# Kernel tuning notes

Hardware: AMD Instinct MI355X
Metric: run time of the kernel (lower is better)

## Reference

```python
import jax, jax.numpy as jnp
import numpy as np

B, S, D = 2, 4096, 768
H, DH = 12, 64
W = 256          # one-sided window (attention_window=512 // 2)
G = 8            # number of global tokens (first G positions)
NEG = -1e9


def setup_inputs() -> dict:
    key = jax.random.key(0)
    ks = jax.random.split(key, 8)
    hidden_states = jax.random.normal(ks[0], (B, S, D), dtype=jnp.float32)
    attention_mask = jnp.ones((B, S), dtype=jnp.float32)
    sc = 0.02
    Wq = jax.random.normal(ks[1], (D, D), dtype=jnp.float32) * sc
    Wk = jax.random.normal(ks[2], (D, D), dtype=jnp.float32) * sc
    Wv = jax.random.normal(ks[3], (D, D), dtype=jnp.float32) * sc
    Wqg = jax.random.normal(ks[4], (D, D), dtype=jnp.float32) * sc
    Wkg = jax.random.normal(ks[5], (D, D), dtype=jnp.float32) * sc
    Wvg = jax.random.normal(ks[6], (D, D), dtype=jnp.float32) * sc
    return {"hidden_states": hidden_states, "attention_mask": attention_mask,
            "Wq": Wq, "Wk": Wk, "Wv": Wv, "Wqg": Wqg, "Wkg": Wkg, "Wvg": Wvg}


def _heads(x):  # [B,S,D] -> [B,H,S,DH]
    return x.reshape(B, S, H, DH).transpose(0, 2, 1, 3)


def longformer_attn(hidden_states, attention_mask, Wq, Wk, Wv, Wqg, Wkg, Wvg):
    scale = 1.0 / jnp.sqrt(jnp.float32(DH))
    q = _heads(hidden_states @ Wq) * scale   # [B,H,S,DH]
    k = _heads(hidden_states @ Wk)
    v = _heads(hidden_states @ Wv)

    n = S // W                                # number of query chunks
    kp = jnp.pad(k, ((0, 0), (0, 0), (W, W), (0, 0)))
    vp = jnp.pad(v, ((0, 0), (0, 0), (W, W), (0, 0)))
    # window indices into padded seq: chunk i covers keys [i*W - W, i*W + 2W)
    idx = jnp.arange(n)[:, None] * W + jnp.arange(3 * W)[None, :]   # [n,3W]
    k_win = kp[:, :, idx]                     # [B,H,n,3W,DH]
    v_win = vp[:, :, idx]
    qc = q.reshape(B, H, n, W, DH)

    scores = jnp.einsum('bhnqd,bhnkd->bhnqk', qc, k_win)  # [B,H,n,W,3W]

    # masks: band (|key-query|<=W), valid key position, not a global key,
    # and key attention_mask
    rel = jnp.arange(3 * W)[None, :] - jnp.arange(W)[:, None]   # [W,3W] = k - q
    band = (rel >= 0) & (rel <= 2 * W)
    key_pos = idx - W                                           # [n,3W] real positions
    valid = (key_pos >= 0) & (key_pos < S) & (key_pos >= G)
    struct_mask = band[None, :, :] & valid[:, None, :]          # [n,W,3W]
    amp = jnp.pad(attention_mask, ((0, 0), (W, W)))
    am_win = amp[:, idx] > 0.5                                  # [B,n,3W]
    full_mask = struct_mask[None] & am_win[:, :, None, :]       # [B,n,W,3W]
    scores = jnp.where(full_mask[:, None], scores, NEG)

    # every query also attends to the G global keys (regular key projection)
    gk = k[:, :, :G]                                            # [B,H,G,DH]
    gscore = jnp.einsum('bhsd,bhgd->bhsg', q, gk).reshape(B, H, n, W, G)
    all_scores = jnp.concatenate([gscore, scores], axis=-1)     # [B,H,n,W,G+3W]
    probs = jax.nn.softmax(all_scores, axis=-1)

    gv = v[:, :, :G]
    out = (jnp.einsum('bhnqk,bhnkd->bhnqd', probs[..., G:], v_win)
           + jnp.einsum('bhnqg,bhgd->bhnqd', probs[..., :G], gv))
    out = out.reshape(B, H, S, DH)

    # global queries attend to ALL tokens with the *_global projections
    qg = _heads(hidden_states @ Wqg)[:, :, :G] * scale          # [B,H,G,DH]
    kg = _heads(hidden_states @ Wkg)
    vg = _heads(hidden_states @ Wvg)
    gs = jnp.einsum('bhgd,bhsd->bhgs', qg, kg)                  # [B,H,G,S]
    gs = jnp.where(attention_mask[:, None, None, :] > 0.5, gs, NEG)
    gp = jax.nn.softmax(gs, axis=-1)
    gout = jnp.einsum('bhgs,bhsd->bhgd', gp, vg)
    out = out.at[:, :, :G].set(gout)

    return out.transpose(0, 2, 1, 3).reshape(B, S, D)


def reference(hidden_states, attention_mask, Wq, Wk, Wv, Wqg, Wkg, Wvg):
    return longformer_attn(hidden_states, attention_mask, Wq, Wk, Wv, Wqg, Wkg, Wvg)
```

## Files before the change

### kernel.cpp

```cpp
#include <hip/hip_runtime.h>

#define B_ 2
#define S_ 4096
#define D_ 768
#define H_ 12
#define DH_ 64
#define W_ 256
#define G_ 8
#define NEG_ (-1e9f)
#define NC_ 64
#define CK_ 64
#define WQB 128
#define NT_ 11

typedef __attribute__((ext_vector_type(4))) float f32x4;
typedef __attribute__((ext_vector_type(16))) float f32x16;
typedef __attribute__((ext_vector_type(8))) short s16x8;
typedef __attribute__((ext_vector_type(4))) short s16x4;
typedef unsigned short ushort_t;

__device__ __forceinline__ unsigned short f2bf(float f) {
    union { float f; unsigned u; } v; v.f = f;
    unsigned r = v.u + 0x7FFFu + ((v.u >> 16) & 1u);
    return (unsigned short)(r >> 16);
}
__device__ __forceinline__ float bf2f(unsigned short b) {
    union { unsigned u; float f; } v; v.u = ((unsigned)b) << 16;
    return v.f;
}
__device__ __forceinline__ unsigned cvtpk_bf16(float lo, float hi) {
    unsigned r;
    asm("v_cvt_pk_bf16_f32 %0, %1, %2" : "=v"(r) : "v"(lo), "v"(hi));
    return r;
}
__device__ __forceinline__ void gload16(const ushort_t* g, ushort_t* l) {
    __builtin_amdgcn_global_load_lds(
        (const __attribute__((address_space(1))) unsigned*)g,
        (__attribute__((address_space(3))) unsigned*)l, 16, 0, 0);
}

__global__ __launch_bounds__(256) void convert_hs(const float* __restrict__ x,
                                                  ushort_t* __restrict__ y, int n8) {
    int i = blockIdx.x * 256 + threadIdx.x;
    if (i >= n8) return;
    float4 a = *(const float4*)&x[(size_t)i * 8];
    float4 c = *(const float4*)&x[(size_t)i * 8 + 4];
    s16x8 o;
    o[0] = (short)f2bf(a.x); o[1] = (short)f2bf(a.y);
    o[2] = (short)f2bf(a.z); o[3] = (short)f2bf(a.w);
    o[4] = (short)f2bf(c.x); o[5] = (short)f2bf(c.y);
    o[6] = (short)f2bf(c.z); o[7] = (short)f2bf(c.w);
    *(s16x8*)&y[(size_t)i * 8] = o;
}

__global__ __launch_bounds__(256) void convert_wt(const float* __restrict__ W0,
                                                  const float* __restrict__ W1,
                                                  const float* __restrict__ W2,
                                                  const float* __restrict__ W3,
                                                  const float* __restrict__ W4,
                                                  ushort_t* __restrict__ wt) {
    __shared__ float tile[32][33];
    const int w = blockIdx.z;
    const float* Wsrc = (w == 0) ? W0 : (w == 1) ? W1 : (w == 2) ? W2 : (w == 3) ? W3 : W4;
    const float scl = (w == 0) ? 0.125f * 1.44269504f : 1.0f;
    const int k0 = blockIdx.x * 32;
    const int n0 = blockIdx.y * 32;
    const int t = threadIdx.x;
    const int r = t >> 3, c4 = (t & 7) * 4;
    float4 src = *(const float4*)&Wsrc[(size_t)(k0 + r) * D_ + n0 + c4];
    tile[r][c4 + 0] = src.x; tile[r][c4 + 1] = src.y;
    tile[r][c4 + 2] = src.z; tile[r][c4 + 3] = src.w;
    __syncthreads();
    s16x4 o;
    o[0] = (short)f2bf(tile[c4 + 0][r] * scl);
    o[1] = (short)f2bf(tile[c4 + 1][r] * scl);
    o[2] = (short)f2bf(tile[c4 + 2][r] * scl);
    o[3] = (short)f2bf(tile[c4 + 3][r] * scl);
    *(s16x4*)&wt[((size_t)(w * D_ + n0 + r)) * D_ + k0 + c4] = o;
}

__global__ __launch_bounds__(256, 2) void proj_mfma(const ushort_t* __restrict__ A,
                                                    const ushort_t* __restrict__ Bt,
                                                    ushort_t* __restrict__ oq,
                                                    ushort_t* __restrict__ ok,
                                                    ushort_t* __restrict__ ov,
                                                    ushort_t* __restrict__ okg,
                                                    ushort_t* __restrict__ ovg) {
    __shared__ char smem[34048];
    ushort_t* Al = (ushort_t*)smem;
    ushort_t* Bl = Al + 128 * 64;

    const int t = threadIdx.x;
    const int m0 = blockIdx.x * 128;
    const int n0 = blockIdx.y * 128;
    const int lane = t & 63;
    const int w = t >> 6;
    const int wm = (w >> 1) * 64, wn = (w & 1) * 64;
    const int ln = lane & 15, hi = lane >> 4;

    const int srow_in_call = lane >> 3;
    const int scol = ((lane & 7) ^ srow_in_call) * 8;

    f32x4 acc[4][4];
#pragma unroll
    for (int mi = 0; mi < 4; ++mi)
#pragma unroll
        for (int ni = 0; ni < 4; ++ni) acc[mi][ni] = (f32x4){0.f, 0.f, 0.f, 0.f};

    for (int k0 = 0; k0 < D_; k0 += 64) {
        __syncthreads();
#pragma unroll
        for (int j = 0; j < 4; ++j) {
            const int rbase = (w * 4 + j) * 8;
            const int row = rbase + srow_in_call;
            gload16(&A[(size_t)(m0 + row) * D_ + k0 + scol], &Al[rbase * 64]);
            gload16(&Bt[(size_t)(n0 + row) * D_ + k0 + scol], &Bl[rbase * 64]);
        }
        __syncthreads();

#pragma unroll
        for (int ks = 0; ks < 2; ++ks) {
            s16x8 af[4], bf[4];
#pragma unroll
            for (int i = 0; i < 4; ++i) {
                const int ar = wm + i * 16 + ln;
                const int br = wn + i * 16 + ln;
                const int slot = (4 * ks + hi) ^ (ln & 7);
                af[i] = *(const s16x8*)&Al[ar * 64 + slot * 8];
                bf[i] = *(const s16x8*)&Bl[br * 64 + slot * 8];
            }
#pragma unroll
            for (int mi = 0; mi < 4; ++mi)
#pragma unroll
                for (int ni = 0; ni < 4; ++ni)
                    acc[mi][ni] = __builtin_amdgcn_mfma_f32_16x16x32_bf16(af[mi], bf[ni], acc[mi][ni], 0, 0, 0);
        }
    }

    float* scr = (float*)smem;
    const int rl = t >> 2, cs = (t & 3) * 32;
    const int ng = n0 + cs;
    const int w_idx = ng / D_;
    const int cb = ng - w_idx * D_;
    const int hh = cb >> 6, dd = cb & 63;
    ushort_t* dst = (w_idx == 0) ? oq : (w_idx == 1) ? ok : (w_idx == 2) ? ov
                    : (w_idx == 3) ? okg : ovg;

#pragma unroll
    for (int r = 0; r < 2; ++r) {
        __syncthreads();
        if ((w >> 1) == r) {
#pragma unroll
            for (int mi = 0; mi < 4; ++mi)
#pragma unroll
                for (int ni = 0; ni < 4; ++ni)
#pragma unroll
                    for (int rr = 0; rr < 4; ++rr)
                        scr[(mi * 16 + hi * 4 + rr) * 132 + wn + ni * 16 + ln] = acc[mi][ni][rr];
        }
        __syncthreads();
        const int m = m0 + r * 64 + rl;
        const int bb = m >> 12, s = m & 4095;
        ushort_t* drow = dst + ((size_t)(bb * H_ + hh) * S_ + s) * DH_ + dd;
        const float* srcp = scr + rl * 132 + cs;
#pragma unroll
        for (int seg = 0; seg < 4; ++seg) {
            float4 lo = *(const float4*)&srcp[seg * 8];
            float4 hi4 = *(const float4*)&srcp[seg * 8 + 4];
            s16x8 o;
            o[0] = (short)f2bf(lo.x); o[1] = (short)f2bf(lo.y);
            o[2] = (short)f2bf(lo.z); o[3] = (short)f2bf(lo.w);
            o[4] = (short)f2bf(hi4.x); o[5] = (short)f2bf(hi4.y);
            o[6] = (short)f2bf(hi4.z); o[7] = (short)f2bf(hi4.w);
            *(s16x8*)&drow[seg * 8] = o;
        }
    }
}

__global__ __launch_bounds__(256) void qg_gemm(const float* __restrict__ X,
                                               const float* __restrict__ Wm,
                                               float* __restrict__ qg) {
    const int rp = blockIdx.x;
    const int c0 = blockIdx.y * 128;
    const int t = threadIdx.x;
    const int r = t >> 7, cl = t & 127;
    __shared__ float xr[2][D_];
    for (int i = t; i < 2 * D_; i += 256) {
        const int rr = i / D_, kk = i - rr * D_;
        const int row = rp * 2 + rr;
        const int b = row >> 3, g = row & 7;
        xr[rr][kk] = X[((size_t)b * S_ + g) * D_ + kk];
    }
    __syncthreads();
    float a0 = 0.f, a1 = 0.f, a2 = 0.f, a3 = 0.f;
    const float* wp = &Wm[c0 + cl];
    for (int kk = 0; kk < D_; kk += 4) {
        a0 += xr[r][kk + 0] * wp[(size_t)(kk + 0) * D_];
        a1 += xr[r][kk + 1] * wp[(size_t)(kk + 1) * D_];
        a2 += xr[r][kk + 2] * wp[(size_t)(kk + 2) * D_];
        a3 += xr[r][kk + 3] * wp[(size_t)(kk + 3) * D_];
    }
    const int row = rp * 2 + r;
    qg[(size_t)row * D_ + c0 + cl] = (a0 + a1 + a2 + a3) * 0.125f;
}

__global__ __launch_bounds__(256, 2) void win_mfma(const ushort_t* __restrict__ q,
                                                   const ushort_t* __restrict__ k,
                                                   const ushort_t* __restrict__ v,
                                                   const float* __restrict__ am,
                                                   float* __restrict__ out) {
    __shared__ char smem[34816];
    ushort_t* Kl = (ushort_t*)smem;
    ushort_t* Vt = Kl + 64 * 72;
    unsigned* Mv = (unsigned*)(Vt + 64 * 66);
    float* Ow = (float*)smem;

    const int n = blockIdx.x, h = blockIdx.y, b = blockIdx.z;
    const int t = threadIdx.x;
    const int lane = t & 63, w = t >> 6;
    const int l31 = lane & 31, h5 = lane >> 5;
    const int q0w = n * WQB + w * 32;
    const int q_abs = q0w + l31;
    const size_t bh = (size_t)(b * H_ + h) * S_;

    s16x8 qf[4];
#pragma unroll
    for (int ks = 0; ks < 4; ++ks)
        qf[ks] = *(const s16x8*)&q[(bh + q_abs) * DH_ + ks * 16 + 8 * h5];

    f32x16 oacc[2];
#pragma unroll
    for (int dt = 0; dt < 2; ++dt)
#pragma unroll
        for (int i = 0; i < 16; ++i) oacc[dt][i] = 0.f;
    float m_run, l_run;

    const int srow = t >> 2, soff = (t & 3) * 16;
    s16x8 kreg0, kreg1, vreg0, vreg1;
    float amv = 0.f;

    {
        const ushort_t* krow = &k[(bh + srow) * DH_ + soff];
        kreg0 = *(const s16x8*)krow;
        kreg1 = *(const s16x8*)(krow + 8);
        const ushort_t* vrow = &v[(bh + srow) * DH_ + soff];
        vreg0 = *(const s16x8*)vrow;
        vreg1 = *(const s16x8*)(vrow + 8);
        *(s16x8*)&Kl[srow * 72 + soff] = kreg0;
        *(s16x8*)&Kl[srow * 72 + soff + 8] = kreg1;
#pragma unroll
        for (int i = 0; i < 8; ++i) {
            Vt[(soff + i) * 66 + srow] = (ushort_t)vreg0[i];
            Vt[(soff + 8 + i) * 66 + srow] = (ushort_t)vreg1[i];
        }
    }
    __syncthreads();

    {
        const int p = n * WQB - W_ + srow;
        const int pr = p < 0 ? 0 : p;
        const ushort_t* krow = &k[(bh + pr) * DH_ + soff];
        kreg0 = *(const s16x8*)krow;
        kreg1 = *(const s16x8*)(krow + 8);
        const ushort_t* vrow = &v[(bh + pr) * DH_ + soff];
        vreg0 = *(const s16x8*)vrow;
        vreg1 = *(const s16x8*)(vrow + 8);
        if (w == 0) {
            const int p2 = n * WQB - W_ + lane;
            amv = (p2 >= 0 && p2 < S_) ? am[(size_t)b * S_ + p2] : 0.f;
        }
    }

    {
        f32x16 s0;
#pragma unroll
        for (int i = 0; i < 16; ++i) s0[i] = 0.f;
#pragma unroll
        for (int ks = 0; ks < 4; ++ks) {
            s16x8 kf = *(const s16x8*)&Kl[l31 * 72 + ks * 16 + 8 * h5];
            s0 = __builtin_amdgcn_mfma_f32_32x32x16_bf16(kf, qf[ks], s0, 0, 0, 0);
        }
        float tmax = fmaxf(fmaxf(s0[0], s0[1]), fmaxf(s0[2], s0[3]));
        tmax = fmaxf(tmax, __shfl_xor(tmax, 32));
        m_run = tmax;
        float p0 = exp2f(s0[0] - m_run), p1 = exp2f(s0[1] - m_run);
        float p2 = exp2f(s0[2] - m_run), p3 = exp2f(s0[3] - m_run);
        float psum = p0 + p1 + p2 + p3;
        psum += __shfl_xor(psum, 32);
        l_run = psum;
        const unsigned Au = cvtpk_bf16(p0, p1);
        const unsigned Bu = cvtpk_bf16(p2, p3);
        const unsigned send0 = h5 ? Au : 0u;
        const unsigned send1 = h5 ? Bu : 0u;
        const unsigned recv0 = __shfl_xor((int)send0, 32);
        const unsigned recv1 = __shfl_xor((int)send1, 32);
        union { unsigned u[4]; s16x8 v8; } pu;
        pu.u[0] = h5 ? recv0 : Au;
        pu.u[1] = h5 ? recv1 : Bu;
        pu.u[2] = h5 ? 0u : recv0;
        pu.u[3] = h5 ? 0u : recv1;
#pragma unroll
        for (int dt = 0; dt < 2; ++dt) {
            const int vbase = (dt * 32 + l31) * 66 + 8 * h5;
            union { unsigned u[4]; s16x8 v8; } vf;
            vf.u[0] = *(const unsigned*)&Vt[vbase + 0];
            vf.u[1] = *(const unsigned*)&Vt[vbase + 2];
            vf.u[2] = *(const unsigned*)&Vt[vbase + 4];
            vf.u[3] = *(const unsigned*)&Vt[vbase + 6];
            oacc[dt] = __builtin_amdgcn_mfma_f32_32x32x16_bf16(vf.v8, pu.v8, oacc[dt], 0, 0, 0);
        }
    }

    for (int tt = 1; tt < NT_; ++tt) {
        const int pbase = n * WQB - W_ + (tt - 1) * 64;
        __syncthreads();
        *(s16x8*)&Kl[srow * 72 + soff] = kreg0;
        *(s16x8*)&Kl[srow * 72 + soff + 8] = kreg1;
#pragma unroll
        for (int i = 0; i < 8; ++i) {
            Vt[(soff + i) * 66 + srow] = (ushort_t)vreg0[i];
            Vt[(soff + 8 + i) * 66 + srow] = (ushort_t)vreg1[i];
        }
        if (w == 0) {
            const int p2 = pbase + lane;
            const bool ok = (p2 >= G_ && p2 < S_ && amv > 0.5f);
            unsigned long long bal = __ballot(ok);
            if (lane == 0) { Mv[0] = (unsigned)bal; Mv[1] = (unsigned)(bal >> 32); }
        }
        __syncthreads();

        if (tt < NT_ - 1) {
            const int p = pbase + 64 + srow;
            const int pr = p < 0 ? 0 : (p >= S_ ? S_ - 1 : p);
            const ushort_t* krow = &k[(bh + pr) * DH_ + soff];
            kreg0 = *(const s16x8*)krow;
            kreg1 = *(const s16x8*)(krow + 8);
            const ushort_t* vrow = &v[(bh + pr) * DH_ + soff];
            vreg0 = *(const s16x8*)vrow;
            vreg1 = *(const s16x8*)(vrow + 8);
            if (w == 0) {
                const int p2 = pbase + 64 + lane;
                amv = (p2 >= 0 && p2 < S_) ? am[(size_t)b * S_ + p2] : 0.f;
            }
        }

        if (pbase > q0w + 31 + W_ || pbase + 63 < q0w - W_) continue;

        f32x16 sc[2];
#pragma unroll
        for (int st = 0; st < 2; ++st)
#pragma unroll
            for (int i = 0; i < 16; ++i) sc[st][i] = 0.f;
#pragma unroll
        for (int st = 0; st < 2; ++st)
#pragma unroll
            for (int ks = 0; ks < 4; ++ks) {
                s16x8 kf = *(const s16x8*)&Kl[(st * 32 + l31) * 72 + ks * 16 + 8 * h5];
                sc[st] = __builtin_amdgcn_mfma_f32_32x32x16_bf16(kf, qf[ks], sc[st], 0, 0, 0);
            }

        const unsigned mv0 = Mv[0], mv1 = Mv[1];
        const bool fullt = ((mv0 & mv1) == 0xFFFFFFFFu) &&
                           (pbase >= q0w + 31 - W_) && (pbase + 63 <= q0w + W_);
        float tmax = -1e30f;
        if (fullt) {
#pragma unroll
            for (int st = 0; st < 2; ++st)
#pragma unroll
                for (int reg = 0; reg < 16; ++reg) tmax = fmaxf(tmax, sc[st][reg]);
        } else {
#pragma unroll
            for (int st = 0; st < 2; ++st)
#pragma unroll
                for (int reg = 0; reg < 16; ++reg) {
                    const int cst = (reg & 3) + 8 * (reg >> 2);
                    const int crow = cst + 4 * h5;
                    const int key_abs = pbase + st * 32 + crow;
                    const unsigned mvx = (st == 0) ? mv0 : mv1;
                    const bool valid = ((mvx >> crow) & 1u) &&
                                       (key_abs >= q_abs - W_) && (key_abs <= q_abs + W_);
                    const float s = valid ? sc[st][reg] : -1e30f;
                    sc[st][reg] = s;
                    tmax = fmaxf(tmax, s);
                }
        }
        tmax = fmaxf(tmax, __shfl_xor(tmax, 32));

        if (__any(tmax > m_run + 11.5f)) {
            const float mnew = fmaxf(m_run, tmax);
            const float f = exp2f(m_run - mnew);
            l_run *= f;
#pragma unroll
            for (int dt = 0; dt < 2; ++dt)
#pragma unroll
                for (int i = 0; i < 16; ++i) oacc[dt][i] *= f;
            m_run = mnew;
        }
        float psum = 0.f;
#pragma unroll
        for (int st = 0; st < 2; ++st)
#pragma unroll
            for (int reg = 0; reg < 16; ++reg) {
                const float p = exp2f(sc[st][reg] - m_run);
                sc[st][reg] = p;
                psum += p;
            }
        psum += __shfl_xor(psum, 32);
        l_run += psum;

#pragma unroll
        for (int ks = 0; ks < 4; ++ks) {
            const int st = ks >> 1, k8 = (ks & 1) * 8;
            const unsigned Au = cvtpk_bf16(sc[st][k8 + 0], sc[st][k8 + 1]);
            const unsigned Bu = cvtpk_bf16(sc[st][k8 + 2], sc[st][k8 + 3]);
            const unsigned Cu = cvtpk_bf16(sc[st][k8 + 4], sc[st][k8 + 5]);
            const unsigned Du = cvtpk_bf16(sc[st][k8 + 6], sc[st][k8 + 7]);
            const unsigned send0 = h5 ? Au : Cu;
            const unsigned send1 = h5 ? Bu : Du;
            const unsigned recv0 = __shfl_xor((int)send0, 32);
            const unsigned recv1 = __shfl_xor((int)send1, 32);
            union { unsigned u[4]; s16x8 v8; } pu;
            pu.u[0] = h5 ? recv0 : Au;
            pu.u[1] = h5 ? recv1 : Bu;
            pu.u[2] = h5 ? Cu : recv0;
            pu.u[3] = h5 ? Du : recv1;
#pragma unroll
            for (int dt = 0; dt < 2; ++dt) {
                const int vbase = (dt * 32 + l31) * 66 + ks * 16 + 8 * h5;
                union { unsigned u[4]; s16x8 v8; } vf;
                vf.u[0] = *(const unsigned*)&Vt[vbase + 0];
                vf.u[1] = *(const unsigned*)&Vt[vbase + 2];
                vf.u[2] = *(const unsigned*)&Vt[vbase + 4];
                vf.u[3] = *(const unsigned*)&Vt[vbase + 6];
                oacc[dt] = __builtin_amdgcn_mfma_f32_32x32x16_bf16(vf.v8, pu.v8, oacc[dt], 0, 0, 0);
            }
        }
    }

    __syncthreads();
    const float inv = 1.0f / l_run;
    float* OwW = Ow + w * 32 * 68;
#pragma unroll
    for (int dt = 0; dt < 2; ++dt)
#pragma unroll
        for (int reg = 0; reg < 16; ++reg) {
            const int d = dt * 32 + (reg & 3) + 8 * (reg >> 2) + 4 * h5;
            OwW[l31 * 68 + d] = oacc[dt][reg] * inv;
        }
    asm volatile("s_waitcnt lgkmcnt(0)" ::: "memory");
    const int qq = lane >> 1, half = lane & 1;
    const float* src = &OwW[qq * 68 + half * 32];
    float* dstp = &out[((size_t)b * S_ + q0w + qq) * D_ + h * DH_ + half * 32];
#pragma unroll
    for (int j = 0; j < 8; ++j)
        *(float4*)&dstp[j * 4] = *(const float4*)&src[j * 4];
}

__global__ __launch_bounds__(256) void glob_partial(const float* __restrict__ qg,
                                                    const ushort_t* __restrict__ kg,
                                                    const ushort_t* __restrict__ vg,
                                                    const float* __restrict__ am,
                                                    float* __restrict__ pout,
                                                    float* __restrict__ pm,
                                                    float* __restrict__ pl) {
    const int c = blockIdx.x, h = blockIdx.y, b = blockIdx.z;
    const int t = threadIdx.x;
    const int bh = b * H_ + h;
    const size_t base = (size_t)bh * S_ * DH_;
    const int jg0 = c * CK_;

    __shared__ float qs[G_][DH_];
    __shared__ float kt[CK_][69];
    __shared__ float vt[CK_][68];
    __shared__ float ps[G_][CK_];

    for (int i = t; i < G_ * DH_; i += 256)
        qs[i >> 6][i & 63] = qg[(size_t)(b * G_ + (i >> 6)) * D_ + h * DH_ + (i & 63)];
    {
        const int row = t >> 2, off = (t & 3) * 16;
        const ushort_t* kr = &kg[base + (size_t)(jg0 + row) * DH_ + off];
        const ushort_t* vr = &vg[base + (size_t)(jg0 + row) * DH_ + off];
        s16x8 ka = *(const s16x8*)kr;
        s16x8 kb2 = *(const s16x8*)(kr + 8);
        s16x8 va = *(const s16x8*)vr;
        s16x8 vb = *(const s16x8*)(vr + 8);
#pragma unroll
        for (int i = 0; i < 8; ++i) {
            kt[row][off + i] = bf2f((ushort_t)ka[i]);
            kt[row][off + 8 + i] = bf2f((ushort_t)kb2[i]);
            vt[row][off + i] = bf2f((ushort_t)va[i]);
            vt[row][off + 8 + i] = bf2f((ushort_t)vb[i]);
        }
    }
    __syncthreads();

    const int g = t >> 5, jl = t & 31;
    float sc0 = 0.f, sc1 = 0.f;
#pragma unroll 8
    for (int d = 0; d < DH_; ++d) {
        const float qv = qs[g][d];
        sc0 += qv * kt[jl][d];
        sc1 += qv * kt[jl + 32][d];
    }
    if (!(am[(size_t)b * S_ + jg0 + jl] > 0.5f)) sc0 = NEG_;
    if (!(am[(size_t)b * S_ + jg0 + jl + 32] > 0.5f)) sc1 = NEG_;

    float mm = fmaxf(sc0, sc1);
    mm = fmaxf(mm, __shfl_xor(mm, 1));
    mm = fmaxf(mm, __shfl_xor(mm, 2));
    mm = fmaxf(mm, __shfl_xor(mm, 4));
    mm = fmaxf(mm, __shfl_xor(mm, 8));
    mm = fmaxf(mm, __shfl_xor(mm, 16));
    const float p0 = __expf(sc0 - mm);
    const float p1 = __expf(sc1 - mm);
    float ls = p0 + p1;
    ls += __shfl_xor(ls, 1);
    ls += __shfl_xor(ls, 2);
    ls += __shfl_xor(ls, 4);
    ls += __shfl_xor(ls, 8);
    ls += __shfl_xor(ls, 16);
    ps[g][jl] = p0;
    ps[g][jl + 32] = p1;
    if (jl == 0) {
        pm[((size_t)bh * NC_ + c) * G_ + g] = mm;
        pl[((size_t)bh * NC_ + c) * G_ + g] = ls;
    }
    __syncthreads();

#pragma unroll
    for (int pass = 0; pass < 2; ++pass) {
        const int gg = (t >> 6) + pass * 4;
        const int d = t & 63;
        float acc = 0.f;
#pragma unroll 8
        for (int j = 0; j < CK_; ++j) acc += ps[gg][j] * vt[j][d];
        pout[(((size_t)bh * NC_ + c) * G_ + gg) * DH_ + d] = acc;
    }
}

__global__ __launch_bounds__(256) void glob_reduce(const float* __restrict__ pout,
                                                   const float* __restrict__ pm,
                                                   const float* __restrict__ pl,
                                                   float* __restrict__ out) {
    const int bh = blockIdx.x;
    const int b = bh / H_, h = bh - b * H_;
    const int t = threadIdx.x;

    __shared__ float wc[G_][NC_];
    __shared__ float wsum[G_];

    const int g = t >> 5, cl = t & 31;
    const float m0 = pm[((size_t)bh * NC_ + cl) * G_ + g];
    const float m1 = pm[((size_t)bh * NC_ + cl + 32) * G_ + g];
    float M = fmaxf(m0, m1);
    M = fmaxf(M, __shfl_xor(M, 1));
    M = fmaxf(M, __shfl_xor(M, 2));
    M = fmaxf(M, __shfl_xor(M, 4));
    M = fmaxf(M, __shfl_xor(M, 8));
    M = fmaxf(M, __shfl_xor(M, 16));
    const float w0 = __expf(m0 - M);
    const float w1 = __expf(m1 - M);
    float S = w0 * pl[((size_t)bh * NC_ + cl) * G_ + g] +
              w1 * pl[((size_t)bh * NC_ + cl + 32) * G_ + g];
    S += __shfl_xor(S, 1);
    S += __shfl_xor(S, 2);
    S += __shfl_xor(S, 4);
    S += __shfl_xor(S, 8);
    S += __shfl_xor(S, 16);
    wc[g][cl] = w0;
    wc[g][cl + 32] = w1;
    if (cl == 0) wsum[g] = S;
    __syncthreads();

#pragma unroll
    for (int pass = 0; pass < 2; ++pass) {
        const int gg = (t >> 6) + pass * 4;
        const int d = t & 63;
        float acc = 0.f;
        for (int c2 = 0; c2 < NC_; ++c2)
            acc += wc[gg][c2] * pout[(((size_t)bh * NC_ + c2) * G_ + gg) * DH_ + d];
        out[((size_t)b * S_ + gg) * D_ + h * DH_ + d] = acc / wsum[gg];
    }
}

extern "C" void kernel_launch(void* const* d_in, const int* in_sizes, int n_in,
                              void* d_out, int out_size, void* d_ws, size_t ws_size,
                              hipStream_t stream) {
    (void)in_sizes; (void)n_in; (void)out_size; (void)ws_size;

    const float* hs    = (const float*)d_in[0];
    const float* amask = (const float*)d_in[1];
    const float* Wq    = (const float*)d_in[2];
    const float* Wk    = (const float*)d_in[3];
    const float* Wv    = (const float*)d_in[4];
    const float* Wqg   = (const float*)d_in[5];
    const float* Wkg   = (const float*)d_in[6];
    const float* Wvg   = (const float*)d_in[7];
    float* out = (float*)d_out;

    char* p = (char*)d_ws;
    ushort_t* hs_bf = (ushort_t*)p; p += (size_t)B_ * S_ * D_ * 2;
    ushort_t* wt    = (ushort_t*)p; p += (size_t)5 * D_ * D_ * 2;
    const size_t per = (size_t)B_ * H_ * S_ * DH_;
    ushort_t* qb  = (ushort_t*)p; p += per * 2;
    ushort_t* kb  = (ushort_t*)p; p += per * 2;
    ushort_t* vb  = (ushort_t*)p; p += per * 2;
    ushort_t* kgb = (ushort_t*)p; p += per * 2;
    ushort_t* vgb = (ushort_t*)p; p += per * 2;
    float* qg   = (float*)p; p += (size_t)B_ * G_ * D_ * 4;
    float* pout = (float*)p; p += (size_t)B_ * H_ * NC_ * G_ * DH_ * 4;
    float* pm   = (float*)p; p += (size_t)B_ * H_ * NC_ * G_ * 4;
    float* pl   = (float*)p;

    convert_hs<<<(B_ * S_ * D_ / 8 + 255) / 256, 256, 0, stream>>>(hs, hs_bf, B_ * S_ * D_ / 8);
    convert_wt<<<dim3(D_ / 32, D_ / 32, 5), 256, 0, stream>>>(Wq, Wk, Wv, Wkg, Wvg, wt);
    proj_mfma<<<dim3(B_ * S_ / 128, 5 * D_ / 128), 256, 0, stream>>>(hs_bf, wt, qb, kb, vb, kgb, vgb);
    qg_gemm<<<dim3(B_ * G_ / 2, D_ / 128), 256, 0, stream>>>(hs, Wqg, qg);
    win_mfma<<<dim3(S_ / WQB, H_, B_), 256, 0, stream>>>(qb, kb, vb, amask, out);
    glob_partial<<<dim3(NC_, H_, B_), 256, 0, stream>>>(qg, kgb, vgb, amask, pout, pm, pl);
    glob_reduce<<<B_ * H_, 256, 0, stream>>>(pout, pm, pl, out);
}
```

Baseline: 157.8 us.

## Fuse preprocessing kernels and shrink windowed attention blocks to 64 queries

Result: slower. 161.0 us (+2.1%).

```diff
diff --git a/kernel.cpp b/kernel.cpp
--- a/kernel.cpp
+++ b/kernel.cpp
@@ -10,8 +10,8 @@
 #define NEG_ (-1e9f)
 #define NC_ 64
 #define CK_ 64
-#define WQB 128
-#define NT_ 11
+#define WQB 64
+#define NT_ 10
 
 typedef __attribute__((ext_vector_type(4))) float f32x4;
 typedef __attribute__((ext_vector_type(16))) float f32x16;
@@ -38,45 +38,88 @@
         (const __attribute__((address_space(1))) unsigned*)g,
         (__attribute__((address_space(3))) unsigned*)l, 16, 0, 0);
 }
-
-__global__ __launch_bounds__(256) void convert_hs(const float* __restrict__ x,
-                                                  ushort_t* __restrict__ y, int n8) {
-    int i = blockIdx.x * 256 + threadIdx.x;
-    if (i >= n8) return;
-    float4 a = *(const float4*)&x[(size_t)i * 8];
-    float4 c = *(const float4*)&x[(size_t)i * 8 + 4];
-    s16x8 o;
-    o[0] = (short)f2bf(a.x); o[1] = (short)f2bf(a.y);
-    o[2] = (short)f2bf(a.z); o[3] = (short)f2bf(a.w);
-    o[4] = (short)f2bf(c.x); o[5] = (short)f2bf(c.y);
-    o[6] = (short)f2bf(c.z); o[7] = (short)f2bf(c.w);
-    *(s16x8*)&y[(size_t)i * 8] = o;
-}
-
-__global__ __launch_bounds__(256) void convert_wt(const float* __restrict__ W0,
-                                                  const float* __restrict__ W1,
-                                                  const float* __restrict__ W2,
-                                                  const float* __restrict__ W3,
-                                                  const float* __restrict__ W4,
-                                                  ushort_t* __restrict__ wt) {
-    __shared__ float tile[32][33];
-    const int w = blockIdx.z;
-    const float* Wsrc = (w == 0) ? W0 : (w == 1) ? W1 : (w == 2) ? W2 : (w == 3) ? W3 : W4;
-    const float scl = (w == 0) ? 0.125f * 1.44269504f : 1.0f;
-    const int k0 = blockIdx.x * 32;
-    const int n0 = blockIdx.y * 32;
+__device__ __forceinline__ float vmax16f(f32x16 v) {
+    float a0 = fmaxf(v[0], v[1]), a1 = fmaxf(v[2], v[3]);
+    float a2 = fmaxf(v[4], v[5]), a3 = fmaxf(v[6], v[7]);
+    float a4 = fmaxf(v[8], v[9]), a5 = fmaxf(v[10], v[11]);
+    float a6 = fmaxf(v[12], v[13]), a7 = fmaxf(v[14], v[15]);
+    return fmaxf(fmaxf(fmaxf(a0, a1), fmaxf(a2, a3)),
+                 fmaxf(fmaxf(a4, a5), fmaxf(a6, a7)));
+}
+__device__ __forceinline__ float vsum16f(f32x16 v) {
+    float a0 = v[0] + v[1], a1 = v[2] + v[3];
+    float a2 = v[4] + v[5], a3 = v[6] + v[7];
+    float a4 = v[8] + v[9], a5 = v[10] + v[11];
+    float a6 = v[12] + v[13], a7 = v[14] + v[15];
+    return ((a0 + a1) + (a2 + a3)) + ((a4 + a5) + (a6 + a7));
+}
+
+__global__ __launch_bounds__(256) void fused_pre(const float* __restrict__ hs,
+                                                 const float* __restrict__ W0,
+                                                 const float* __restrict__ W1,
+                                                 const float* __restrict__ W2,
+                                                 const float* __restrict__ W3,
+                                                 const float* __restrict__ W4,
+                                                 const float* __restrict__ Wqg,
+                                                 ushort_t* __restrict__ hs_bf,
+                                                 ushort_t* __restrict__ wt,
+                                                 float* __restrict__ qg) {
+    __shared__ float smf[2 * D_];
+    const int bid = blockIdx.x;
     const int t = threadIdx.x;
-    const int r = t >> 3, c4 = (t & 7) * 4;
-    float4 src = *(const float4*)&Wsrc[(size_t)(k0 + r) * D_ + n0 + c4];
-    tile[r][c4 + 0] = src.x; tile[r][c4 + 1] = src.y;
-    tile[r][c4 + 2] = src.z; tile[r][c4 + 3] = src.w;
-    __syncthreads();
-    s16x4 o;
-    o[0] = (short)f2bf(tile[c4 + 0][r] * scl);
-    o[1] = (short)f2bf(tile[c4 + 1][r] * scl);
-    o[2] = (short)f2bf(tile[c4 + 2][r] * scl);
-    o[3] = (short)f2bf(tile[c4 + 3][r] * scl);
-    *(s16x4*)&wt[((size_t)(w * D_ + n0 + r)) * D_ + k0 + c4] = o;
+
+    if (bid < 3072) {
+        const int i = bid * 256 + t;
+        float4 a = *(const float4*)&hs[(size_t)i * 8];
+        float4 c = *(const float4*)&hs[(size_t)i * 8 + 4];
+        s16x8 o;
+        o[0] = (short)f2bf(a.x); o[1] = (short)f2bf(a.y);
+        o[2] = (short)f2bf(a.z); o[3] = (short)f2bf(a.w);
+        o[4] = (short)f2bf(c.x); o[5] = (short)f2bf(c.y);
+        o[6] = (short)f2bf(c.z); o[7] = (short)f2bf(c.w);
+        *(s16x8*)&hs_bf[(size_t)i * 8] = o;
+    } else if (bid < 5952) {
+        const int bid2 = bid - 3072;
+        const int w = bid2 / 576;
+        const int rem = bid2 - w * 576;
+        const int k0 = (rem / 24) * 32;
+        const int n0 = (rem % 24) * 32;
+        const float* Wsrc = (w == 0) ? W0 : (w == 1) ? W1 : (w == 2) ? W2 : (w == 3) ? W3 : W4;
+        const float scl = (w == 0) ? 0.125f * 1.44269504f : 1.0f;
+        const int r = t >> 3, c4 = (t & 7) * 4;
+        float4 src = *(const float4*)&Wsrc[(size_t)(k0 + r) * D_ + n0 + c4];
+        smf[r * 33 + c4 + 0] = src.x; smf[r * 33 + c4 + 1] = src.y;
+        smf[r * 33 + c4 + 2] = src.z; smf[r * 33 + c4 + 3] = src.w;
+        __syncthreads();
+        s16x4 o;
+        o[0] = (short)f2bf(smf[(c4 + 0) * 33 + r] * scl);
+        o[1] = (short)f2bf(smf[(c4 + 1) * 33 + r] * scl);
+        o[2] = (short)f2bf(smf[(c4 + 2) * 33 + r] * scl);
+        o[3] = (short)f2bf(smf[(c4 + 3) * 33 + r] * scl);
+        *(s16x4*)&wt[((size_t)(w * D_ + n0 + r)) * D_ + k0 + c4] = o;
+    } else {
+        const int bid3 = bid - 5952;
+        const int rp = bid3 / 6;
+        const int c0 = (bid3 - rp * 6) * 128;
+        const int r = t >> 7, cl = t & 127;
+        for (int i = t; i < 2 * D_; i += 256) {
+            const int rr = i / D_, kk = i - rr * D_;
+            const int row = rp * 2 + rr;
+            const int b = row >> 3, g = row & 7;
+            smf[rr * D_ + kk] = hs[((size_t)b * S_ + g) * D_ + kk];
+        }
+        __syncthreads();
+        float a0 = 0.f, a1 = 0.f, a2 = 0.f, a3 = 0.f;
+        const float* wp = &Wqg[c0 + cl];
+        for (int kk = 0; kk < D_; kk += 4) {
+            a0 += smf[r * D_ + kk + 0] * wp[(size_t)(kk + 0) * D_];
+            a1 += smf[r * D_ + kk + 1] * wp[(size_t)(kk + 1) * D_];
+            a2 += smf[r * D_ + kk + 2] * wp[(size_t)(kk + 2) * D_];
+            a3 += smf[r * D_ + kk + 3] * wp[(size_t)(kk + 3) * D_];
+        }
+        const int row = rp * 2 + r;
+        qg[(size_t)row * D_ + c0 + cl] = (a0 + a1 + a2 + a3) * 0.125f;
+    }
 }
 
 __global__ __launch_bounds__(256, 2) void proj_mfma(const ushort_t* __restrict__ A,
@@ -177,39 +220,12 @@
     }
 }
 
-__global__ __launch_bounds__(256) void qg_gemm(const float* __restrict__ X,
-                                               const float* __restrict__ Wm,
-                                               float* __restrict__ qg) {
-    const int rp = blockIdx.x;
-    const int c0 = blockIdx.y * 128;
-    const int t = threadIdx.x;
-    const int r = t >> 7, cl = t & 127;
-    __shared__ float xr[2][D_];
-    for (int i = t; i < 2 * D_; i += 256) {
-        const int rr = i / D_, kk = i - rr * D_;
-        const int row = rp * 2 + rr;
-        const int b = row >> 3, g = row & 7;
-        xr[rr][kk] = X[((size_t)b * S_ + g) * D_ + kk];
-    }
-    __syncthreads();
-    float a0 = 0.f, a1 = 0.f, a2 = 0.f, a3 = 0.f;
-    const float* wp = &Wm[c0 + cl];
-    for (int kk = 0; kk < D_; kk += 4) {
-        a0 += xr[r][kk + 0] * wp[(size_t)(kk + 0) * D_];
-        a1 += xr[r][kk + 1] * wp[(size_t)(kk + 1) * D_];
-        a2 += xr[r][kk + 2] * wp[(size_t)(kk + 2) * D_];
-        a3 += xr[r][kk + 3] * wp[(size_t)(kk + 3) * D_];
-    }
-    const int row = rp * 2 + r;
-    qg[(size_t)row * D_ + c0 + cl] = (a0 + a1 + a2 + a3) * 0.125f;
-}
-
-__global__ __launch_bounds__(256, 2) void win_mfma(const ushort_t* __restrict__ q,
+__global__ __launch_bounds__(128, 2) void win_mfma(const ushort_t* __restrict__ q,
                                                    const ushort_t* __restrict__ k,
                                                    const ushort_t* __restrict__ v,
                                                    const float* __restrict__ am,
                                                    float* __restrict__ out) {
-    __shared__ char smem[34816];
+    __shared__ char smem[17680];
     ushort_t* Kl = (ushort_t*)smem;
     ushort_t* Vt = Kl + 64 * 72;
     unsigned* Mv = (unsigned*)(Vt + 64 * 66);
@@ -235,23 +251,27 @@
         for (int i = 0; i < 16; ++i) oacc[dt][i] = 0.f;
     float m_run, l_run;
 
-    const int srow = t >> 2, soff = (t & 3) * 16;
-    s16x8 kreg0, kreg1, vreg0, vreg1;
+    const int srow = t >> 1, soff = (t & 1) * 32;
+    s16x8 kr0, kr1, kr2, kr3, vr0, vr1, vr2, vr3;
     float amv = 0.f;
 
     {
         const ushort_t* krow = &k[(bh + srow) * DH_ + soff];
-        kreg0 = *(const s16x8*)krow;
-        kreg1 = *(const s16x8*)(krow + 8);
+        kr0 = *(const s16x8*)krow;       kr1 = *(const s16x8*)(krow + 8);
+        kr2 = *(const s16x8*)(krow + 16); kr3 = *(const s16x8*)(krow + 24);
         const ushort_t* vrow = &v[(bh + srow) * DH_ + soff];
-        vreg0 = *(const s16x8*)vrow;
-        vreg1 = *(const s16x8*)(vrow + 8);
-        *(s16x8*)&Kl[srow * 72 + soff] = kreg0;
-        *(s16x8*)&Kl[srow * 72 + soff + 8] = kreg1;
+        vr0 = *(const s16x8*)vrow;       vr1 = *(const s16x8*)(vrow + 8);
+        vr2 = *(const s16x8*)(vrow + 16); vr3 = *(const s16x8*)(vrow + 24);
+        *(s16x8*)&Kl[srow * 72 + soff] = kr0;
+        *(s16x8*)&Kl[srow * 72 + soff + 8] = kr1;
+        *(s16x8*)&Kl[srow * 72 + soff + 16] = kr2;
+        *(s16x8*)&Kl[srow * 72 + soff + 24] = kr3;
 #pragma unroll
         for (int i = 0; i < 8; ++i) {
-            Vt[(soff + i) * 66 + srow] = (ushort_t)vreg0[i];
-            Vt[(soff + 8 + i) * 66 + srow] = (ushort_t)vreg1[i];
+            Vt[(soff + i) * 66 + srow] = (ushort_t)vr0[i];
+            Vt[(soff + 8 + i) * 66 + srow] = (ushort_t)vr1[i];
+            Vt[(soff + 16 + i) * 66 + srow] = (ushort_t)vr2[i];
+            Vt[(soff + 24 + i) * 66 + srow] = (ushort_t)vr3[i];
         }
     }
     __syncthreads();
@@ -260,11 +280,11 @@
         const int p = n * WQB - W_ + srow;
         const int pr = p < 0 ? 0 : p;
         const ushort_t* krow = &k[(bh + pr) * DH_ + soff];
-        kreg0 = *(const s16x8*)krow;
-        kreg1 = *(const s16x8*)(krow + 8);
+        kr0 = *(const s16x8*)krow;       kr1 = *(const s16x8*)(krow + 8);
+        kr2 = *(const s16x8*)(krow + 16); kr3 = *(const s16x8*)(krow + 24);
         const ushort_t* vrow = &v[(bh + pr) * DH_ + soff];
-        vreg0 = *(const s16x8*)vrow;
-        vreg1 = *(const s16x8*)(vrow + 8);
+        vr0 = *(const s16x8*)vrow;       vr1 = *(const s16x8*)(vrow + 8);
+        vr2 = *(const s16x8*)(vrow + 16); vr3 = *(const s16x8*)(vrow + 24);
         if (w == 0) {
             const int p2 = n * WQB - W_ + lane;
             amv = (p2 >= 0 && p2 < S_) ? am[(size_t)b * S_ + p2] : 0.f;
@@ -285,7 +305,7 @@
         m_run = tmax;
         float p0 = exp2f(s0[0] - m_run), p1 = exp2f(s0[1] - m_run);
         float p2 = exp2f(s0[2] - m_run), p3 = exp2f(s0[3] - m_run);
-        float psum = p0 + p1 + p2 + p3;
+        float psum = (p0 + p1) + (p2 + p3);
         psum += __shfl_xor(psum, 32);
         l_run = psum;
         const unsigned Au = cvtpk_bf16(p0, p1);
@@ -314,12 +334,16 @@
     for (int tt = 1; tt < NT_; ++tt) {
         const int pbase = n * WQB - W_ + (tt - 1) * 64;
         __syncthreads();
-        *(s16x8*)&Kl[srow * 72 + soff] = kreg0;
-        *(s16x8*)&Kl[srow * 72 + soff + 8] = kreg1;
+        *(s16x8*)&Kl[srow * 72 + soff] = kr0;
+        *(s16x8*)&Kl[srow * 72 + soff + 8] = kr1;
+        *(s16x8*)&Kl[srow * 72 + soff + 16] = kr2;
+        *(s16x8*)&Kl[srow * 72 + soff + 24] = kr3;
 #pragma unroll
         for (int i = 0; i < 8; ++i) {
-            Vt[(soff + i) * 66 + srow] = (ushort_t)vreg0[i];
-            Vt[(soff + 8 + i) * 66 + srow] = (ushort_t)vreg1[i];
+            Vt[(soff + i) * 66 + srow] = (ushort_t)vr0[i];
+            Vt[(soff + 8 + i) * 66 + srow] = (ushort_t)vr1[i];
+            Vt[(soff + 16 + i) * 66 + srow] = (ushort_t)vr2[i];
+            Vt[(soff + 24 + i) * 66 + srow] = (ushort_t)vr3[i];
         }
         if (w == 0) {
             const int p2 = pbase + lane;
@@ -333,19 +357,17 @@
             const int p = pbase + 64 + srow;
             const int pr = p < 0 ? 0 : (p >= S_ ? S_ - 1 : p);
             const ushort_t* krow = &k[(bh + pr) * DH_ + soff];
-            kreg0 = *(const s16x8*)krow;
-            kreg1 = *(const s16x8*)(krow + 8);
+            kr0 = *(const s16x8*)krow;       kr1 = *(const s16x8*)(krow + 8);
+            kr2 = *(const s16x8*)(krow + 16); kr3 = *(const s16x8*)(krow + 24);
             const ushort_t* vrow = &v[(bh + pr) * DH_ + soff];
-            vreg0 = *(const s16x8*)vrow;
-            vreg1 = *(const s16x8*)(vrow + 8);
+            vr0 = *(const s16x8*)vrow;       vr1 = *(const s16x8*)(vrow + 8);
+            vr2 = *(const s16x8*)(vrow + 16); vr3 = *(const s16x8*)(vrow + 24);
             if (w == 0) {
                 const int p2 = pbase + 64 + lane;
                 amv = (p2 >= 0 && p2 < S_) ? am[(size_t)b * S_ + p2] : 0.f;
             }
         }
 
-        if (pbase > q0w + 31 + W_ || pbase + 63 < q0w - W_) continue;
-
         f32x16 sc[2];
 #pragma unroll
         for (int st = 0; st < 2; ++st)
@@ -362,13 +384,7 @@
         const unsigned mv0 = Mv[0], mv1 = Mv[1];
         const bool fullt = ((mv0 & mv1) == 0xFFFFFFFFu) &&
                            (pbase >= q0w + 31 - W_) && (pbase + 63 <= q0w + W_);
-        float tmax = -1e30f;
-        if (fullt) {
-#pragma unroll
-            for (int st = 0; st < 2; ++st)
-#pragma unroll
-                for (int reg = 0; reg < 16; ++reg) tmax = fmaxf(tmax, sc[st][reg]);
-        } else {
+        if (!fullt) {
 #pragma unroll
             for (int st = 0; st < 2; ++st)
 #pragma unroll
@@ -379,11 +395,10 @@
                     const unsigned mvx = (st == 0) ? mv0 : mv1;
                     const bool valid = ((mvx >> crow) & 1u) &&
                                        (key_abs >= q_abs - W_) && (key_abs <= q_abs + W_);
-                    const float s = valid ? sc[st][reg] : -1e30f;
-                    sc[st][reg] = s;
-                    tmax = fmaxf(tmax, s);
+                    sc[st][reg] = valid ? sc[st][reg] : -1e30f;
                 }
         }
+        float tmax = fmaxf(vmax16f(sc[0]), vmax16f(sc[1]));
         tmax = fmaxf(tmax, __shfl_xor(tmax, 32));
 
         if (__any(tmax > m_run + 11.5f)) {
@@ -396,15 +411,12 @@
                 for (int i = 0; i < 16; ++i) oacc[dt][i] *= f;
             m_run = mnew;
         }
-        float psum = 0.f;
 #pragma unroll
         for (int st = 0; st < 2; ++st)
 #pragma unroll
-            for (int reg = 0; reg < 16; ++reg) {
-                const float p = exp2f(sc[st][reg] - m_run);
-                sc[st][reg] = p;
-                psum += p;
-            }
+            for (int reg = 0; reg < 16; ++reg)
+                sc[st][reg] = exp2f(sc[st][reg] - m_run);
+        float psum = vsum16f(sc[0]) + vsum16f(sc[1]);
         psum += __shfl_xor(psum, 32);
         l_run += psum;
 
@@ -612,11 +624,9 @@
     float* pm   = (float*)p; p += (size_t)B_ * H_ * NC_ * G_ * 4;
     float* pl   = (float*)p;
 
-    convert_hs<<<(B_ * S_ * D_ / 8 + 255) / 256, 256, 0, stream>>>(hs, hs_bf, B_ * S_ * D_ / 8);
-    convert_wt<<<dim3(D_ / 32, D_ / 32, 5), 256, 0, stream>>>(Wq, Wk, Wv, Wkg, Wvg, wt);
+    fused_pre<<<6000, 256, 0, stream>>>(hs, Wq, Wk, Wv, Wkg, Wvg, Wqg, hs_bf, wt, qg);
     proj_mfma<<<dim3(B_ * S_ / 128, 5 * D_ / 128), 256, 0, stream>>>(hs_bf, wt, qb, kb, vb, kgb, vgb);
-    qg_gemm<<<dim3(B_ * G_ / 2, D_ / 128), 256, 0, stream>>>(hs, Wqg, qg);
-    win_mfma<<<dim3(S_ / WQB, H_, B_), 256, 0, stream>>>(qb, kb, vb, amask, out);
+    win_mfma<<<dim3(S_ / WQB, H_, B_), 128, 0, stream>>>(qb, kb, vb, amask, out);
     glob_partial<<<dim3(NC_, H_, B_), 256, 0, stream>>>(qg, kgb, vgb, amask, pout, pm, pl);
     glob_reduce<<<B_ * H_, 256, 0, stream>>>(pout, pm, pl, out);
 }
```
